# Performance work log

Measured on AMD Instinct MI355X. Metric: run time of the kernel, lower is better.

Reference implementation:

```python
import jax, jax.numpy as jnp
import numpy as np

B, N, K = 4, 40960, 16
D_IN, D_OUT = 32, 64


def setup_inputs() -> dict:
    key = jax.random.key(0)
    keys = iter(jax.random.split(key, 48))
    def nrm(shape, scale):
        return (jax.random.normal(next(keys), shape, jnp.float32) * scale).astype(jnp.float32)
    inp = {
        "feature": jax.random.normal(next(keys), (B, N, D_IN), jnp.float32),
        "xyz": jax.random.uniform(next(keys), (B, N, 3), jnp.float32),
        "neigh_idx": jax.random.randint(next(keys), (B, N, K), 0, N, jnp.int32),
    }
    def conv_bn(name, cin, cout):
        inp["w_" + name] = nrm((cin, cout), (2.0 / cin) ** 0.5)
        inp["s_" + name] = 1.0 + nrm((cout,), 0.1)  # folded BN scale: gamma/sqrt(var+eps)
        inp["b_" + name] = nrm((cout,), 0.1)        # folded BN bias: beta - mean*scale
    conv_bn("mlp1", D_IN, D_OUT // 2)
    conv_bn("lfa1", 10, D_OUT // 2)
    inp["w_att1_fc"] = nrm((D_OUT, D_OUT), (2.0 / D_OUT) ** 0.5)
    conv_bn("att1_mlp", D_OUT, D_OUT // 2)
    conv_bn("lfa2", D_OUT // 2, D_OUT // 2)
    inp["w_att2_fc"] = nrm((D_OUT, D_OUT), (2.0 / D_OUT) ** 0.5)
    conv_bn("att2_mlp", D_OUT, D_OUT)
    conv_bn("mlp2", D_OUT, 2 * D_OUT)
    conv_bn("sc", D_IN, 2 * D_OUT)
    return inp


def _gather(pc, idx):
    # pc: [B,N,D], idx: [B,N,K] -> [B,N,K,D]
    b, n, k = idx.shape
    flat = jnp.take_along_axis(pc, idx.reshape(b, n * k, 1), axis=1)
    return flat.reshape(b, n, k, pc.shape[-1])


def _cb(x, w, s, b, relu=True):
    # 1x1 conv + folded BN (+ ReLU), channels-last
    y = jnp.einsum('...i,io->...o', x, w) * s + b
    return jnp.maximum(y, 0.0) if relu else y


def _att_pool(fs, w_fc, w, s, b):
    # fs: [B,N,K,C]; softmax-attention pooling over K, then mlp
    scores = jax.nn.softmax(jnp.einsum('bnkc,cd->bnkd', fs, w_fc), axis=2)
    agg = jnp.sum(fs * scores, axis=2)  # [B,N,C]
    return _cb(agg, w, s, b)


def _rel_pos(xyz, idx):
    nbr = _gather(xyz, idx)                           # [B,N,K,3]
    tile = jnp.broadcast_to(xyz[:, :, None, :], nbr.shape)
    rel = tile - nbr
    dist = jnp.sqrt(jnp.sum(rel * rel, axis=-1, keepdims=True))
    return jnp.concatenate([dist, rel, tile, nbr], axis=-1)  # [B,N,K,10]


def reference(feature, xyz, neigh_idx,
              w_mlp1, s_mlp1, b_mlp1,
              w_lfa1, s_lfa1, b_lfa1,
              w_att1_fc, w_att1_mlp, s_att1_mlp, b_att1_mlp,
              w_lfa2, s_lfa2, b_lfa2,
              w_att2_fc, w_att2_mlp, s_att2_mlp, b_att2_mlp,
              w_mlp2, s_mlp2, b_mlp2,
              w_sc, s_sc, b_sc):
    f_pc = _cb(feature, w_mlp1, s_mlp1, b_mlp1)                   # [B,N,d/2]
    f_xyz = _cb(_rel_pos(xyz, neigh_idx), w_lfa1, s_lfa1, b_lfa1)  # [B,N,K,d/2]
    f_nb = _gather(f_pc, neigh_idx)                                # [B,N,K,d/2]
    f_agg = _att_pool(jnp.concatenate([f_nb, f_xyz], axis=-1),
                      w_att1_fc, w_att1_mlp, s_att1_mlp, b_att1_mlp)  # [B,N,d/2]
    f_xyz2 = _cb(f_xyz, w_lfa2, s_lfa2, b_lfa2)                    # [B,N,K,d/2]
    f_nb2 = _gather(f_agg, neigh_idx)                              # [B,N,K,d/2]
    f_pc2 = _att_pool(jnp.concatenate([f_nb2, f_xyz2], axis=-1),
                      w_att2_fc, w_att2_mlp, s_att2_mlp, b_att2_mlp)  # [B,N,d]
    out = _cb(f_pc2, w_mlp2, s_mlp2, b_mlp2, relu=False)           # [B,N,2d]
    sc = _cb(feature, w_sc, s_sc, b_sc, relu=False)
    return jax.nn.leaky_relu(out + sc, negative_slope=0.2)
```

## Files before the change

### kernel.cpp

```cpp
#include <hip/hip_runtime.h>
#include <hip/hip_bf16.h>

#define NPTS  40960
#define BNPTS 163840
#define KNB   16

using bf16x8 = __attribute__((ext_vector_type(8))) short;
using f32x4  = __attribute__((ext_vector_type(4))) float;

__device__ __forceinline__ unsigned short f2bf(float x) {
    union { float f; unsigned u; } v; v.f = x;
    unsigned r = v.u + 0x7fffu + ((v.u >> 16) & 1u);
    return (unsigned short)(r >> 16);
}
__device__ __forceinline__ float bf2f(unsigned short u) {
    union { unsigned u; float f; } v; v.u = ((unsigned)u) << 16;
    return v.f;
}
__device__ __forceinline__ unsigned pk2(float lo, float hi) {
    union { __hip_bfloat162 h; unsigned u; } v;
    v.h = __float22bfloat162_rn(float2{lo, hi});
    return v.u;
}
__device__ __forceinline__ bf16x8 pack8(float a0, float a1, float a2, float a3,
                                        float a4, float a5, float a6, float a7) {
    union { unsigned u[4]; bf16x8 v; } w;
    w.u[0] = pk2(a0, a1); w.u[1] = pk2(a2, a3);
    w.u[2] = pk2(a4, a5); w.u[3] = pk2(a6, a7);
    return w.v;
}
__device__ __forceinline__ f32x4 mfma16(bf16x8 a, bf16x8 b, f32x4 c) {
    return __builtin_amdgcn_mfma_f32_16x16x32_bf16(a, b, c, 0, 0, 0);
}
__device__ __forceinline__ float exp2_fast(float x) { return __builtin_amdgcn_exp2f(x); }
__device__ __forceinline__ float rcp_fast(float x)  { return __builtin_amdgcn_rcpf(x); }

__global__ __launch_bounds__(256)
void k_mlp1(const float* __restrict__ feature, const float* __restrict__ w,
            const float* __restrict__ s, const float* __restrict__ b,
            unsigned short* __restrict__ f_pc)
{
    __shared__ unsigned short wT[32 * 40];
    __shared__ float sS[32], sB[32];
    const int tid = threadIdx.x;
    for (int t = tid; t < 1024; t += 256) {
        int c = t >> 5, d = t & 31;
        wT[d * 40 + c] = f2bf(w[t]);
    }
    if (tid < 32) { sS[tid] = s[tid]; sB[tid] = b[tid]; }
    __syncthreads();
    const int lid = tid & 63, wv = tid >> 6;
    const int col = lid & 15, quad = lid >> 4;
    bf16x8 B0 = *(const bf16x8*)&wT[col * 40 + quad * 8];
    bf16x8 B1 = *(const bf16x8*)&wT[(16 + col) * 40 + quad * 8];
    float s0 = sS[col], b0 = sB[col], s1 = sS[16 + col], b1 = sB[16 + col];
    for (int itp = 0; itp < 4; itp++) {
        const int p0 = blockIdx.x * 256 + wv * 64 + itp * 16;
        const float* fr = &feature[(size_t)(p0 + col) * 32 + quad * 8];
        float4 u0 = *(const float4*)fr;
        float4 u1 = *(const float4*)(fr + 4);
        bf16x8 a = pack8(u0.x, u0.y, u0.z, u0.w, u1.x, u1.y, u1.z, u1.w);
        f32x4 z = {0.f, 0.f, 0.f, 0.f};
        f32x4 d0 = mfma16(a, B0, z);
        f32x4 d1 = mfma16(a, B1, z);
        #pragma unroll
        for (int r = 0; r < 4; r++) {
            int p = p0 + quad * 4 + r;
            f_pc[(size_t)p * 32 + col]      = f2bf(fmaxf(d0[r] * s0 + b0, 0.f));
            f_pc[(size_t)p * 32 + 16 + col] = f2bf(fmaxf(d1[r] * s1 + b1, 0.f));
        }
    }
}

template<int NOUT, bool HAS_LFA2>
__global__ __launch_bounds__(256, 4)
void k_att(const float* __restrict__ xyz, const int* __restrict__ nidx,
           const unsigned short* __restrict__ src,
           const float* __restrict__ wlfa1, const float* __restrict__ slfa1, const float* __restrict__ blfa1,
           const float* __restrict__ wlfa2, const float* __restrict__ slfa2, const float* __restrict__ blfa2,
           const float* __restrict__ wfc,
           const float* __restrict__ wmlp, const float* __restrict__ smlp, const float* __restrict__ bmlp,
           unsigned short* __restrict__ out)
{
    constexpr int NP = NOUT / 32;
    constexpr int WS = 88;
    constexpr int WMT_B = (NOUT == 64) ? NOUT * WS * 2 : 0;
    constexpr int U_SIZE = 16384;
    __shared__ __align__(16) char smem[WMT_B + U_SIZE];
    unsigned short* wmT = (unsigned short*)smem;
    char* uni = smem + WMT_B;

    const int tid = threadIdx.x;
    const int lid = tid & 63, wv = tid >> 6;
    const int col = lid & 15, quad = lid >> 4;

    {
        unsigned short* wfcS = (unsigned short*)uni;
        for (int t = tid; t < 64 * 64; t += 256) {
            int c = t >> 6, d = t & 63;
            wfcS[d * WS + c] = f2bf(wfc[t] * 1.4426950408889634f);
        }
        if (NOUT == 64) {
            for (int t = tid; t < 64 * NOUT; t += 256) {
                int c = t / NOUT, d = t % NOUT;
                int slot = (d >> 5) * 32 + (d & 1) * 16 + ((d & 31) >> 1);
                wmT[slot * WS + c] = f2bf(wmlp[t]);
            }
        }
    }
    __syncthreads();
    bf16x8 Bfc[4][2];
    {
        const unsigned short* wfcS = (const unsigned short*)uni;
        #pragma unroll
        for (int nt = 0; nt < 4; nt++)
            #pragma unroll
            for (int ks = 0; ks < 2; ks++)
                Bfc[nt][ks] = *(const bf16x8*)&wfcS[(nt * 16 + col) * WS + ks * 32 + quad * 8];
    }
    __syncthreads();

    {
        unsigned short* wl1S = (unsigned short*)uni;
        unsigned short* wl2S = (unsigned short*)(uni + 2560);
        float* sl2S = (float*)(uni + 5120);
        float* bl2S = sl2S + 32;
        float* smlS = (float*)(uni + 5632);
        float* bmlS = smlS + NOUT;
        for (int t = tid; t < 32 * 32; t += 256) {
            int k = t >> 5, d = t & 31;
            int slot = (d & 1) * 16 + (d >> 1);
            float v1 = k < 10 ? wlfa1[k * 32 + d] * slfa1[d] : (k == 10 ? blfa1[d] : 0.f);
            wl1S[slot * 40 + k] = f2bf(v1);
            if (HAS_LFA2) wl2S[slot * 40 + k] = f2bf(wlfa2[k * 32 + d]);
        }
        if (HAS_LFA2 && tid < 32) { sl2S[tid] = slfa2[tid]; bl2S[tid] = blfa2[tid]; }
        if (tid < NOUT) { smlS[tid] = smlp[tid]; bmlS[tid] = bmlp[tid]; }
    }
    __syncthreads();
    bf16x8 Bl1e, Bl1o, Bl2e{}, Bl2o{};
    float sl2e = 0.f, bl2e = 0.f, sl2o = 0.f, bl2o = 0.f;
    float sme[NP], bme[NP], smo[NP], bmo[NP];
    {
        const unsigned short* wl1S = (const unsigned short*)uni;
        const unsigned short* wl2S = (const unsigned short*)(uni + 2560);
        const float* sl2S = (const float*)(uni + 5120);
        const float* bl2S = sl2S + 32;
        const float* smlS = (const float*)(uni + 5632);
        const float* bmlS = smlS + NOUT;
        Bl1e = *(const bf16x8*)&wl1S[col * 40 + quad * 8];
        Bl1o = *(const bf16x8*)&wl1S[(16 + col) * 40 + quad * 8];
        if (HAS_LFA2) {
            Bl2e = *(const bf16x8*)&wl2S[col * 40 + quad * 8];
            Bl2o = *(const bf16x8*)&wl2S[(16 + col) * 40 + quad * 8];
            sl2e = sl2S[2 * col]; bl2e = bl2S[2 * col];
            sl2o = sl2S[2 * col + 1]; bl2o = bl2S[2 * col + 1];
        }
        #pragma unroll
        for (int tp = 0; tp < NP; tp++) {
            sme[tp] = smlS[tp * 32 + 2 * col]; bme[tp] = bmlS[tp * 32 + 2 * col];
            smo[tp] = smlS[tp * 32 + 2 * col + 1]; bmo[tp] = bmlS[tp * 32 + 2 * col + 1];
        }
    }
    __syncthreads();

    bf16x8 Bme_r[NP][2], Bmo_r[NP][2];
    if constexpr (NOUT == 32) {
        unsigned short* wmS = (unsigned short*)uni;
        for (int t = tid; t < 64 * NOUT; t += 256) {
            int c = t / NOUT, d = t % NOUT;
            int slot = (d >> 5) * 32 + (d & 1) * 16 + ((d & 31) >> 1);
            wmS[slot * WS + c] = f2bf(wmlp[t]);
        }
        __syncthreads();
        #pragma unroll
        for (int tp = 0; tp < NP; tp++)
            #pragma unroll
            for (int ks = 0; ks < 2; ks++) {
                Bme_r[tp][ks] = *(const bf16x8*)&wmS[(tp * 32 + col) * WS + ks * 32 + quad * 8];
                Bmo_r[tp][ks] = *(const bf16x8*)&wmS[(tp * 32 + 16 + col) * WS + ks * 32 + quad * 8];
            }
        __syncthreads();
    }

    unsigned short* fc  = (unsigned short*)(uni) + wv * (16 * WS);
    unsigned short* ag  = (unsigned short*)(uni + 11264) + wv * (4 * 72);
    unsigned short* nb  = (unsigned short*)(uni + 13568) + wv * 256;
    float*          cxy = (float*)(uni + 15616) + wv * 48;

    const int blk = (int)blockIdx.x;
    const int vblk = (blk & 7) * 320 + (blk >> 3);
    const int pbase = vblk * 64 + wv * 16;
    const int pb = (pbase / NPTS) * NPTS;
    const unsigned short* srcb = src + (size_t)pb * 32;
    const float* xyzb = xyz + (size_t)pb * 3;

    {
        int4 t4 = *(const int4*)&nidx[(size_t)pbase * KNB + lid * 4];
        ushort4 u = make_ushort4((unsigned short)t4.x, (unsigned short)t4.y,
                                 (unsigned short)t4.z, (unsigned short)t4.w);
        *(ushort4*)&nb[lid * 4] = u;
        if (lid < 48) cxy[lid] = xyz[(size_t)pbase * 3 + lid];
    }

    const f32x4 z = {0.f, 0.f, 0.f, 0.f};
    bf16x8 vs; float nx = 0.f, ny = 0.f, nz = 0.f;
    {
        int j = (int)nb[col];
        vs = *(const bf16x8*)(srcb + (size_t)j * 32 + quad * 8);
        if (quad < 2) { const float* xp = xyzb + (size_t)j * 3; nx = xp[0]; ny = xp[1]; nz = xp[2]; }
    }

    #pragma unroll 1
    for (int it = 0; it < 16; it++) {
        const int p = pbase + it;
        bf16x8 a0 = vs;
        *(bf16x8*)&fc[col * WS + quad * 8] = a0;

        float cx = cxy[it * 3], cy = cxy[it * 3 + 1], cz = cxy[it * 3 + 2];
        float rx = cx - nx, ry = cy - ny, rz = cz - nz;
        float dd = sqrtf(rx * rx + ry * ry + rz * rz);
        float f0 = 0.f, f1 = 0.f, f2 = 0.f, f3 = 0.f, f4 = 0.f, f5 = 0.f, f6 = 0.f, f7 = 0.f;
        if (quad == 0)      { f0 = dd; f1 = rx; f2 = ry; f3 = rz; f4 = cx; f5 = cy; f6 = cz; f7 = nx; }
        else if (quad == 1) { f0 = ny; f1 = nz; f2 = 1.0f; }
        bf16x8 al = pack8(f0, f1, f2, f3, f4, f5, f6, f7);

        {
            int itn = it < 15 ? it + 1 : 15;
            int j = (int)nb[itn * 16 + col];
            vs = *(const bf16x8*)(srcb + (size_t)j * 32 + quad * 8);
            if (quad < 2) { const float* xp = xyzb + (size_t)j * 3; nx = xp[0]; ny = xp[1]; nz = xp[2]; }
        }

        {
            f32x4 d0 = mfma16(al, Bl1e, z);
            f32x4 d1 = mfma16(al, Bl1o, z);
            #pragma unroll
            for (int r = 0; r < 4; r++) {
                float ye = fmaxf(d0[r], 0.f);
                float yo = fmaxf(d1[r], 0.f);
                *(unsigned*)&fc[(quad * 4 + r) * WS + 32 + 2 * col] = pk2(ye, yo);
            }
            if (HAS_LFA2) {
                bf16x8 a2 = *(const bf16x8*)&fc[col * WS + 32 + quad * 8];
                f32x4 e0 = mfma16(a2, Bl2e, z);
                f32x4 e1 = mfma16(a2, Bl2o, z);
                #pragma unroll
                for (int r = 0; r < 4; r++) {
                    float ye = fmaxf(e0[r] * sl2e + bl2e, 0.f);
                    float yo = fmaxf(e1[r] * sl2o + bl2o, 0.f);
                    *(unsigned*)&fc[(quad * 4 + r) * WS + 32 + 2 * col] = pk2(ye, yo);
                }
            }
        }

        {
            bf16x8 a1 = *(const bf16x8*)&fc[col * WS + 32 + quad * 8];
            #pragma unroll
            for (int nt = 0; nt < 4; nt++) {
                f32x4 L = mfma16(a1, Bfc[nt][1], mfma16(a0, Bfc[nt][0], z));
                float e0 = exp2_fast(L[0]), e1 = exp2_fast(L[1]);
                float e2 = exp2_fast(L[2]), e3 = exp2_fast(L[3]);
                float sden = (e0 + e1) + (e2 + e3);
                const unsigned short* frr = &fc[quad * 4 * WS + nt * 16 + col];
                float av = e0 * bf2f(frr[0]) + e1 * bf2f(frr[WS]) + e2 * bf2f(frr[2 * WS]) + e3 * bf2f(frr[3 * WS]);
                av   += __shfl_xor(av, 16, 64);
                sden += __shfl_xor(sden, 16, 64);
                av   += __shfl_xor(av, 32, 64);
                sden += __shfl_xor(sden, 32, 64);
                if (quad == 0) ag[(it & 3) * 72 + nt * 16 + col] = f2bf(av * rcp_fast(sden));
            }
        }

        if ((it & 3) == 3) {
            bf16x8 am0 = *(const bf16x8*)&ag[(col & 3) * 72 + quad * 8];
            bf16x8 am1 = *(const bf16x8*)&ag[(col & 3) * 72 + 32 + quad * 8];
            #pragma unroll
            for (int tp = 0; tp < NP; tp++) {
                bf16x8 Be0, Be1, Bo0, Bo1;
                if constexpr (NOUT == 32) {
                    Be0 = Bme_r[tp][0]; Be1 = Bme_r[tp][1];
                    Bo0 = Bmo_r[tp][0]; Bo1 = Bmo_r[tp][1];
                } else {
                    Be0 = *(const bf16x8*)&wmT[(tp * 32 + col) * WS + quad * 8];
                    Be1 = *(const bf16x8*)&wmT[(tp * 32 + col) * WS + 32 + quad * 8];
                    Bo0 = *(const bf16x8*)&wmT[(tp * 32 + 16 + col) * WS + quad * 8];
                    Bo1 = *(const bf16x8*)&wmT[(tp * 32 + 16 + col) * WS + 32 + quad * 8];
                }
                f32x4 de = mfma16(am1, Be1, mfma16(am0, Be0, z));
                f32x4 dq = mfma16(am1, Bo1, mfma16(am0, Bo0, z));
                if (quad == 0) {
                    #pragma unroll
                    for (int r = 0; r < 4; r++) {
                        float ye = fmaxf(de[r] * sme[tp] + bme[tp], 0.f);
                        float yo = fmaxf(dq[r] * smo[tp] + bmo[tp], 0.f);
                        *(unsigned*)&out[(size_t)(p - 3 + r) * NOUT + tp * 32 + 2 * col] = pk2(ye, yo);
                    }
                }
            }
        }
    }
}

__global__ __launch_bounds__(256)
void k_out(const unsigned short* __restrict__ f_pc2, const float* __restrict__ feature,
           const float* __restrict__ w2, const float* __restrict__ s2, const float* __restrict__ b2,
           const float* __restrict__ wsc, const float* __restrict__ ssc, const float* __restrict__ bsc,
           float* __restrict__ out)
{
    __shared__ unsigned short w2T[128 * 88];
    __shared__ unsigned short wsT[128 * 40];
    __shared__ float sA[128], sB2[128], sC[128];
    const int tid = threadIdx.x;
    for (int t = tid; t < 64 * 128; t += 256) {
        int c = t >> 7, d = t & 127;
        w2T[d * 88 + c] = f2bf(w2[t]);
    }
    for (int t = tid; t < 32 * 128; t += 256) {
        int c = t >> 7, d = t & 127;
        wsT[d * 40 + c] = f2bf(wsc[t]);
    }
    if (tid < 128) { sA[tid] = s2[tid]; sB2[tid] = ssc[tid]; sC[tid] = b2[tid] + bsc[tid]; }
    __syncthreads();
    const int lid = tid & 63, wv = tid >> 6;
    const int col = lid & 15, quad = lid >> 4;
    const f32x4 z = {0.f, 0.f, 0.f, 0.f};
    #pragma unroll 1
    for (int itp = 0; itp < 2; itp++) {
        const int p0 = blockIdx.x * 128 + wv * 32 + itp * 16;
        const unsigned short* ar = &f_pc2[(size_t)(p0 + col) * 64 + quad * 8];
        bf16x8 a10 = *(const bf16x8*)ar;
        bf16x8 a11 = *(const bf16x8*)(ar + 32);
        const float* fr = &feature[(size_t)(p0 + col) * 32 + quad * 8];
        float4 u0 = *(const float4*)fr;
        float4 u1 = *(const float4*)(fr + 4);
        bf16x8 a2 = pack8(u0.x, u0.y, u0.z, u0.w, u1.x, u1.y, u1.z, u1.w);
        #pragma unroll
        for (int nt = 0; nt < 8; nt++) {
            bf16x8 bk0 = *(const bf16x8*)&w2T[(nt * 16 + col) * 88 + quad * 8];
            bf16x8 bk1 = *(const bf16x8*)&w2T[(nt * 16 + col) * 88 + 32 + quad * 8];
            bf16x8 bs  = *(const bf16x8*)&wsT[(nt * 16 + col) * 40 + quad * 8];
            f32x4 d = mfma16(a11, bk1, mfma16(a10, bk0, z));
            f32x4 e = mfma16(a2, bs, z);
            int n = nt * 16 + col;
            float ss = sA[n], st = sB2[n], bb = sC[n];
            #pragma unroll
            for (int r = 0; r < 4; r++) {
                float y = d[r] * ss + e[r] * st + bb;
                y = y > 0.f ? y : 0.2f * y;
                out[(size_t)(p0 + quad * 4 + r) * 128 + n] = y;
            }
        }
    }
}

extern "C" void kernel_launch(void* const* d_in, const int* in_sizes, int n_in,
                              void* d_out, int out_size, void* d_ws, size_t ws_size,
                              hipStream_t stream) {
    const float* feature = (const float*)d_in[0];
    const float* xyz     = (const float*)d_in[1];
    const int*   nidx    = (const int*)d_in[2];
    const float* w_mlp1 = (const float*)d_in[3];
    const float* s_mlp1 = (const float*)d_in[4];
    const float* b_mlp1 = (const float*)d_in[5];
    const float* w_lfa1 = (const float*)d_in[6];
    const float* s_lfa1 = (const float*)d_in[7];
    const float* b_lfa1 = (const float*)d_in[8];
    const float* w_att1_fc  = (const float*)d_in[9];
    const float* w_att1_mlp = (const float*)d_in[10];
    const float* s_att1_mlp = (const float*)d_in[11];
    const float* b_att1_mlp = (const float*)d_in[12];
    const float* w_lfa2 = (const float*)d_in[13];
    const float* s_lfa2 = (const float*)d_in[14];
    const float* b_lfa2 = (const float*)d_in[15];
    const float* w_att2_fc  = (const float*)d_in[16];
    const float* w_att2_mlp = (const float*)d_in[17];
    const float* s_att2_mlp = (const float*)d_in[18];
    const float* b_att2_mlp = (const float*)d_in[19];
    const float* w_mlp2 = (const float*)d_in[20];
    const float* s_mlp2 = (const float*)d_in[21];
    const float* b_mlp2 = (const float*)d_in[22];
    const float* w_sc = (const float*)d_in[23];
    const float* s_sc = (const float*)d_in[24];
    const float* b_sc = (const float*)d_in[25];

    unsigned short* f_pc  = (unsigned short*)d_ws;
    unsigned short* f_agg = f_pc  + (size_t)BNPTS * 32;
    unsigned short* f_pc2 = f_agg + (size_t)BNPTS * 32;
    float* out = (float*)d_out;

    k_mlp1<<<BNPTS / 256, 256, 0, stream>>>(feature, w_mlp1, s_mlp1, b_mlp1, f_pc);
    k_att<32, false><<<BNPTS / 64, 256, 0, stream>>>(
        xyz, nidx, f_pc,
        w_lfa1, s_lfa1, b_lfa1,
        w_lfa1, s_lfa1, b_lfa1,
        w_att1_fc, w_att1_mlp, s_att1_mlp, b_att1_mlp, f_agg);
    k_att<64, true><<<BNPTS / 64, 256, 0, stream>>>(
        xyz, nidx, f_agg,
        w_lfa1, s_lfa1, b_lfa1,
        w_lfa2, s_lfa2, b_lfa2,
        w_att2_fc, w_att2_mlp, s_att2_mlp, b_att2_mlp, f_pc2);
    k_out<<<BNPTS / 128, 256, 0, stream>>>(
        f_pc2, feature,
        w_mlp2, s_mlp2, b_mlp2,
        w_sc, s_sc, b_sc, out);
}
```

Measured before the change: 375.2 us.

## Pre-pack bf16 weights once in a prep kernel and read them from global memory

Adds a small k_prep kernel that converts and transposes every weight matrix to bf16 once into a packed workspace buffer. The mlp1, attention and output kernels then drop their per-block shared-memory weight staging and syncs, reading the B fragments straight from global memory (k_att<64> now reads wmT from global inside the hot loop). This cuts redundant per-block conversion work and LDS use, at the cost of one extra launch and weight reads that now depend on L1/L2 hits. The k_out inner loop unroll is also reduced to 2.

Measured after the change: 364.7 us. -2.8%, faster.

```diff
diff --git a/kernel.cpp b/kernel.cpp
--- a/kernel.cpp
+++ b/kernel.cpp
@@ -4,6 +4,17 @@
 #define NPTS  40960
 #define BNPTS 163840
 #define KNB   16
+
+#define PK_MLP1 0
+#define PK_FC1  1280
+#define PK_FC2  6912
+#define PK_L1   12544
+#define PK_L2   13824
+#define PK_M1   15104
+#define PK_M2   17920
+#define PK_W2   23552
+#define PK_WS   34816
+#define PK_TOTAL 39936
 
 using bf16x8 = __attribute__((ext_vector_type(8))) short;
 using f32x4  = __attribute__((ext_vector_type(4))) float;
@@ -36,24 +47,84 @@
 __device__ __forceinline__ float rcp_fast(float x)  { return __builtin_amdgcn_rcpf(x); }
 
 __global__ __launch_bounds__(256)
-void k_mlp1(const float* __restrict__ feature, const float* __restrict__ w,
+void k_prep(const float* __restrict__ wm1, const float* __restrict__ wfc1,
+            const float* __restrict__ wfc2,
+            const float* __restrict__ wlfa1, const float* __restrict__ slfa1, const float* __restrict__ blfa1,
+            const float* __restrict__ wlfa2,
+            const float* __restrict__ wam1, const float* __restrict__ wam2,
+            const float* __restrict__ w2, const float* __restrict__ wsc,
+            unsigned short* __restrict__ pk)
+{
+    const int tid = threadIdx.x, blk = blockIdx.x;
+    const float LOG2E = 1.4426950408889634f;
+    switch (blk) {
+    case 0:
+        for (int t = tid; t < 32 * 32; t += 256) {
+            int c = t >> 5, d = t & 31;
+            pk[PK_MLP1 + d * 40 + c] = f2bf(wm1[t]);
+        }
+        break;
+    case 1:
+        for (int t = tid; t < 64 * 64; t += 256) {
+            int c = t >> 6, d = t & 63;
+            pk[PK_FC1 + d * 88 + c] = f2bf(wfc1[t] * LOG2E);
+        }
+        break;
+    case 2:
+        for (int t = tid; t < 64 * 64; t += 256) {
+            int c = t >> 6, d = t & 63;
+            pk[PK_FC2 + d * 88 + c] = f2bf(wfc2[t] * LOG2E);
+        }
+        break;
+    case 3:
+        for (int t = tid; t < 32 * 32; t += 256) {
+            int k = t >> 5, d = t & 31;
+            int slot = (d & 1) * 16 + (d >> 1);
+            float v1 = k < 10 ? wlfa1[k * 32 + d] * slfa1[d] : (k == 10 ? blfa1[d] : 0.f);
+            pk[PK_L1 + slot * 40 + k] = f2bf(v1);
+            pk[PK_L2 + slot * 40 + k] = f2bf(wlfa2[k * 32 + d]);
+        }
+        break;
+    case 4:
+        for (int t = tid; t < 64 * 32; t += 256) {
+            int c = t / 32, d = t % 32;
+            int slot = (d & 1) * 16 + (d >> 1);
+            pk[PK_M1 + slot * 88 + c] = f2bf(wam1[t]);
+        }
+        break;
+    case 5:
+        for (int t = tid; t < 64 * 64; t += 256) {
+            int c = t >> 6, d = t & 63;
+            int slot = (d >> 5) * 32 + (d & 1) * 16 + ((d & 31) >> 1);
+            pk[PK_M2 + slot * 88 + c] = f2bf(wam2[t]);
+        }
+        break;
+    case 6:
+        for (int t = tid; t < 64 * 128; t += 256) {
+            int c = t >> 7, d = t & 127;
+            pk[PK_W2 + d * 88 + c] = f2bf(w2[t]);
+        }
+        break;
+    case 7:
+        for (int t = tid; t < 32 * 128; t += 256) {
+            int c = t >> 7, d = t & 127;
+            pk[PK_WS + d * 40 + c] = f2bf(wsc[t]);
+        }
+        break;
+    }
+}
+
+__global__ __launch_bounds__(256)
+void k_mlp1(const float* __restrict__ feature, const unsigned short* __restrict__ pk,
             const float* __restrict__ s, const float* __restrict__ b,
             unsigned short* __restrict__ f_pc)
 {
-    __shared__ unsigned short wT[32 * 40];
-    __shared__ float sS[32], sB[32];
     const int tid = threadIdx.x;
-    for (int t = tid; t < 1024; t += 256) {
-        int c = t >> 5, d = t & 31;
-        wT[d * 40 + c] = f2bf(w[t]);
-    }
-    if (tid < 32) { sS[tid] = s[tid]; sB[tid] = b[tid]; }
-    __syncthreads();
     const int lid = tid & 63, wv = tid >> 6;
     const int col = lid & 15, quad = lid >> 4;
-    bf16x8 B0 = *(const bf16x8*)&wT[col * 40 + quad * 8];
-    bf16x8 B1 = *(const bf16x8*)&wT[(16 + col) * 40 + quad * 8];
-    float s0 = sS[col], b0 = sB[col], s1 = sS[16 + col], b1 = sB[16 + col];
+    bf16x8 B0 = *(const bf16x8*)&pk[PK_MLP1 + col * 40 + quad * 8];
+    bf16x8 B1 = *(const bf16x8*)&pk[PK_MLP1 + (16 + col) * 40 + quad * 8];
+    float s0 = s[col], b0 = b[col], s1 = s[16 + col], b1 = b[16 + col];
     for (int itp = 0; itp < 4; itp++) {
         const int p0 = blockIdx.x * 256 + wv * 64 + itp * 16;
         const float* fr = &feature[(size_t)(p0 + col) * 32 + quad * 8];
@@ -76,111 +147,50 @@
 __global__ __launch_bounds__(256, 4)
 void k_att(const float* __restrict__ xyz, const int* __restrict__ nidx,
            const unsigned short* __restrict__ src,
-           const float* __restrict__ wlfa1, const float* __restrict__ slfa1, const float* __restrict__ blfa1,
-           const float* __restrict__ wlfa2, const float* __restrict__ slfa2, const float* __restrict__ blfa2,
-           const float* __restrict__ wfc,
-           const float* __restrict__ wmlp, const float* __restrict__ smlp, const float* __restrict__ bmlp,
+           const unsigned short* __restrict__ wl1T, const unsigned short* __restrict__ wl2T,
+           const float* __restrict__ slfa2, const float* __restrict__ blfa2,
+           const unsigned short* __restrict__ wfcT, const unsigned short* __restrict__ wmT,
+           const float* __restrict__ smlp, const float* __restrict__ bmlp,
            unsigned short* __restrict__ out)
 {
     constexpr int NP = NOUT / 32;
     constexpr int WS = 88;
-    constexpr int WMT_B = (NOUT == 64) ? NOUT * WS * 2 : 0;
-    constexpr int U_SIZE = 16384;
-    __shared__ __align__(16) char smem[WMT_B + U_SIZE];
-    unsigned short* wmT = (unsigned short*)smem;
-    char* uni = smem + WMT_B;
+    __shared__ __align__(16) char smem[16384];
+    char* uni = smem;
 
     const int tid = threadIdx.x;
     const int lid = tid & 63, wv = tid >> 6;
     const int col = lid & 15, quad = lid >> 4;
 
-    {
-        unsigned short* wfcS = (unsigned short*)uni;
-        for (int t = tid; t < 64 * 64; t += 256) {
-            int c = t >> 6, d = t & 63;
-            wfcS[d * WS + c] = f2bf(wfc[t] * 1.4426950408889634f);
-        }
-        if (NOUT == 64) {
-            for (int t = tid; t < 64 * NOUT; t += 256) {
-                int c = t / NOUT, d = t % NOUT;
-                int slot = (d >> 5) * 32 + (d & 1) * 16 + ((d & 31) >> 1);
-                wmT[slot * WS + c] = f2bf(wmlp[t]);
-            }
-        }
-    }
-    __syncthreads();
     bf16x8 Bfc[4][2];
-    {
-        const unsigned short* wfcS = (const unsigned short*)uni;
+    #pragma unroll
+    for (int nt = 0; nt < 4; nt++)
         #pragma unroll
-        for (int nt = 0; nt < 4; nt++)
-            #pragma unroll
-            for (int ks = 0; ks < 2; ks++)
-                Bfc[nt][ks] = *(const bf16x8*)&wfcS[(nt * 16 + col) * WS + ks * 32 + quad * 8];
-    }
-    __syncthreads();
-
-    {
-        unsigned short* wl1S = (unsigned short*)uni;
-        unsigned short* wl2S = (unsigned short*)(uni + 2560);
-        float* sl2S = (float*)(uni + 5120);
-        float* bl2S = sl2S + 32;
-        float* smlS = (float*)(uni + 5632);
-        float* bmlS = smlS + NOUT;
-        for (int t = tid; t < 32 * 32; t += 256) {
-            int k = t >> 5, d = t & 31;
-            int slot = (d & 1) * 16 + (d >> 1);
-            float v1 = k < 10 ? wlfa1[k * 32 + d] * slfa1[d] : (k == 10 ? blfa1[d] : 0.f);
-            wl1S[slot * 40 + k] = f2bf(v1);
-            if (HAS_LFA2) wl2S[slot * 40 + k] = f2bf(wlfa2[k * 32 + d]);
-        }
-        if (HAS_LFA2 && tid < 32) { sl2S[tid] = slfa2[tid]; bl2S[tid] = blfa2[tid]; }
-        if (tid < NOUT) { smlS[tid] = smlp[tid]; bmlS[tid] = bmlp[tid]; }
-    }
-    __syncthreads();
-    bf16x8 Bl1e, Bl1o, Bl2e{}, Bl2o{};
+        for (int ks = 0; ks < 2; ks++)
+            Bfc[nt][ks] = *(const bf16x8*)&wfcT[(nt * 16 + col) * WS + ks * 32 + quad * 8];
+    bf16x8 Bl1e = *(const bf16x8*)&wl1T[col * 40 + quad * 8];
+    bf16x8 Bl1o = *(const bf16x8*)&wl1T[(16 + col) * 40 + quad * 8];
+    bf16x8 Bl2e{}, Bl2o{};
     float sl2e = 0.f, bl2e = 0.f, sl2o = 0.f, bl2o = 0.f;
+    if (HAS_LFA2) {
+        Bl2e = *(const bf16x8*)&wl2T[col * 40 + quad * 8];
+        Bl2o = *(const bf16x8*)&wl2T[(16 + col) * 40 + quad * 8];
+        sl2e = slfa2[2 * col]; bl2e = blfa2[2 * col];
+        sl2o = slfa2[2 * col + 1]; bl2o = blfa2[2 * col + 1];
+    }
     float sme[NP], bme[NP], smo[NP], bmo[NP];
-    {
-        const unsigned short* wl1S = (const unsigned short*)uni;
-        const unsigned short* wl2S = (const unsigned short*)(uni + 2560);
-        const float* sl2S = (const float*)(uni + 5120);
-        const float* bl2S = sl2S + 32;
-        const float* smlS = (const float*)(uni + 5632);
-        const float* bmlS = smlS + NOUT;
-        Bl1e = *(const bf16x8*)&wl1S[col * 40 + quad * 8];
-        Bl1o = *(const bf16x8*)&wl1S[(16 + col) * 40 + quad * 8];
-        if (HAS_LFA2) {
-            Bl2e = *(const bf16x8*)&wl2S[col * 40 + quad * 8];
-            Bl2o = *(const bf16x8*)&wl2S[(16 + col) * 40 + quad * 8];
-            sl2e = sl2S[2 * col]; bl2e = bl2S[2 * col];
-            sl2o = sl2S[2 * col + 1]; bl2o = bl2S[2 * col + 1];
-        }
+    #pragma unroll
+    for (int tp = 0; tp < NP; tp++) {
+        sme[tp] = smlp[tp * 32 + 2 * col]; bme[tp] = bmlp[tp * 32 + 2 * col];
+        smo[tp] = smlp[tp * 32 + 2 * col + 1]; bmo[tp] = bmlp[tp * 32 + 2 * col + 1];
+    }
+    bf16x8 Bme_r[2], Bmo_r[2];
+    if constexpr (NOUT == 32) {
         #pragma unroll
-        for (int tp = 0; tp < NP; tp++) {
-            sme[tp] = smlS[tp * 32 + 2 * col]; bme[tp] = bmlS[tp * 32 + 2 * col];
-            smo[tp] = smlS[tp * 32 + 2 * col + 1]; bmo[tp] = bmlS[tp * 32 + 2 * col + 1];
-        }
-    }
-    __syncthreads();
-
-    bf16x8 Bme_r[NP][2], Bmo_r[NP][2];
-    if constexpr (NOUT == 32) {
-        unsigned short* wmS = (unsigned short*)uni;
-        for (int t = tid; t < 64 * NOUT; t += 256) {
-            int c = t / NOUT, d = t % NOUT;
-            int slot = (d >> 5) * 32 + (d & 1) * 16 + ((d & 31) >> 1);
-            wmS[slot * WS + c] = f2bf(wmlp[t]);
-        }
-        __syncthreads();
-        #pragma unroll
-        for (int tp = 0; tp < NP; tp++)
-            #pragma unroll
-            for (int ks = 0; ks < 2; ks++) {
-                Bme_r[tp][ks] = *(const bf16x8*)&wmS[(tp * 32 + col) * WS + ks * 32 + quad * 8];
-                Bmo_r[tp][ks] = *(const bf16x8*)&wmS[(tp * 32 + 16 + col) * WS + ks * 32 + quad * 8];
-            }
-        __syncthreads();
+        for (int ks = 0; ks < 2; ks++) {
+            Bme_r[ks] = *(const bf16x8*)&wmT[col * WS + ks * 32 + quad * 8];
+            Bmo_r[ks] = *(const bf16x8*)&wmT[(16 + col) * WS + ks * 32 + quad * 8];
+        }
     }
 
     unsigned short* fc  = (unsigned short*)(uni) + wv * (16 * WS);
@@ -279,8 +289,8 @@
             for (int tp = 0; tp < NP; tp++) {
                 bf16x8 Be0, Be1, Bo0, Bo1;
                 if constexpr (NOUT == 32) {
-                    Be0 = Bme_r[tp][0]; Be1 = Bme_r[tp][1];
-                    Bo0 = Bmo_r[tp][0]; Bo1 = Bmo_r[tp][1];
+                    Be0 = Bme_r[0]; Be1 = Bme_r[1];
+                    Bo0 = Bmo_r[0]; Bo1 = Bmo_r[1];
                 } else {
                     Be0 = *(const bf16x8*)&wmT[(tp * 32 + col) * WS + quad * 8];
                     Be1 = *(const bf16x8*)&wmT[(tp * 32 + col) * WS + 32 + quad * 8];
@@ -304,26 +314,19 @@
 
 __global__ __launch_bounds__(256)
 void k_out(const unsigned short* __restrict__ f_pc2, const float* __restrict__ feature,
-           const float* __restrict__ w2, const float* __restrict__ s2, const float* __restrict__ b2,
-           const float* __restrict__ wsc, const float* __restrict__ ssc, const float* __restrict__ bsc,
+           const unsigned short* __restrict__ pk,
+           const float* __restrict__ s2, const float* __restrict__ b2,
+           const float* __restrict__ ssc, const float* __restrict__ bsc,
            float* __restrict__ out)
 {
-    __shared__ unsigned short w2T[128 * 88];
-    __shared__ unsigned short wsT[128 * 40];
     __shared__ float sA[128], sB2[128], sC[128];
     const int tid = threadIdx.x;
-    for (int t = tid; t < 64 * 128; t += 256) {
-        int c = t >> 7, d = t & 127;
-        w2T[d * 88 + c] = f2bf(w2[t]);
-    }
-    for (int t = tid; t < 32 * 128; t += 256) {
-        int c = t >> 7, d = t & 127;
-        wsT[d * 40 + c] = f2bf(wsc[t]);
-    }
     if (tid < 128) { sA[tid] = s2[tid]; sB2[tid] = ssc[tid]; sC[tid] = b2[tid] + bsc[tid]; }
     __syncthreads();
     const int lid = tid & 63, wv = tid >> 6;
     const int col = lid & 15, quad = lid >> 4;
+    const unsigned short* w2T = pk + PK_W2;
+    const unsigned short* wsT = pk + PK_WS;
     const f32x4 z = {0.f, 0.f, 0.f, 0.f};
     #pragma unroll 1
     for (int itp = 0; itp < 2; itp++) {
@@ -335,7 +338,7 @@
         float4 u0 = *(const float4*)fr;
         float4 u1 = *(const float4*)(fr + 4);
         bf16x8 a2 = pack8(u0.x, u0.y, u0.z, u0.w, u1.x, u1.y, u1.z, u1.w);
-        #pragma unroll
+        #pragma unroll 2
         for (int nt = 0; nt < 8; nt++) {
             bf16x8 bk0 = *(const bf16x8*)&w2T[(nt * 16 + col) * 88 + quad * 8];
             bf16x8 bk1 = *(const bf16x8*)&w2T[(nt * 16 + col) * 88 + 32 + quad * 8];
@@ -387,21 +390,24 @@
     unsigned short* f_pc  = (unsigned short*)d_ws;
     unsigned short* f_agg = f_pc  + (size_t)BNPTS * 32;
     unsigned short* f_pc2 = f_agg + (size_t)BNPTS * 32;
+    unsigned short* pkw   = f_pc2 + (size_t)BNPTS * 64;
     float* out = (float*)d_out;
 
-    k_mlp1<<<BNPTS / 256, 256, 0, stream>>>(feature, w_mlp1, s_mlp1, b_mlp1, f_pc);
+    k_prep<<<8, 256, 0, stream>>>(w_mlp1, w_att1_fc, w_att2_fc,
+                                  w_lfa1, s_lfa1, b_lfa1, w_lfa2,
+                                  w_att1_mlp, w_att2_mlp, w_mlp2, w_sc, pkw);
+    k_mlp1<<<BNPTS / 256, 256, 0, stream>>>(feature, pkw, s_mlp1, b_mlp1, f_pc);
     k_att<32, false><<<BNPTS / 64, 256, 0, stream>>>(
         xyz, nidx, f_pc,
-        w_lfa1, s_lfa1, b_lfa1,
-        w_lfa1, s_lfa1, b_lfa1,
-        w_att1_fc, w_att1_mlp, s_att1_mlp, b_att1_mlp, f_agg);
+        pkw + PK_L1, pkw + PK_L1,
+        s_lfa1, b_lfa1,
+        pkw + PK_FC1, pkw + PK_M1, s_att1_mlp, b_att1_mlp, f_agg);
     k_att<64, true><<<BNPTS / 64, 256, 0, stream>>>(
         xyz, nidx, f_agg,
-        w_lfa1, s_lfa1, b_lfa1,
-        w_lfa2, s_lfa2, b_lfa2,
-        w_att2_fc, w_att2_mlp, s_att2_mlp, b_att2_mlp, f_pc2);
+        pkw + PK_L1, pkw + PK_L2,
+        s_lfa2, b_lfa2,
+        pkw + PK_FC2, pkw + PK_M2, s_att2_mlp, b_att2_mlp, f_pc2);
     k_out<<<BNPTS / 128, 256, 0, stream>>>(
-        f_pc2, feature,
-        w_mlp2, s_mlp2, b_mlp2,
-        w_sc, s_sc, b_sc, out);
-}
+        f_pc2, feature, pkw,
+        s_mlp2, b_mlp2, s_sc, b_sc, out);
+}
```
